# Performance work log

Measured on AMD Instinct MI355X. Metric: run time of the kernel, lower is better.

## Reference

```python
import jax, jax.numpy as jnp
import numpy as np


def setup_inputs() -> dict:
    key = jax.random.key(0)
    k1, k2 = jax.random.split(key)
    B, H, W, C = 16, 1024, 1024, 3
    image = jax.random.normal(k1, (B, H, W, C), dtype=jnp.float32)
    flow = jax.random.normal(k2, (B, H, W, 2), dtype=jnp.float32)
    return {"image": image, "flow": flow}


def reference(image, flow):
    # Backward warp: out(p) = bilinear_sample(image, p + flow(p)).
    # NOTE: the original build() swaps width/height (width=shape[1], height=shape[2]);
    # this is only consistent for square images (H == W), which we assume here.
    B, H, W, C = image.shape
    grid_x = jnp.arange(W, dtype=jnp.float32)[None, None, :]  # [1,1,W]
    grid_y = jnp.arange(H, dtype=jnp.float32)[None, :, None]  # [1,H,1]
    x = grid_x + flow[..., 0]  # [B,H,W]
    y = grid_y + flow[..., 1]
    # normalize to [-1,1] then back (faithful to original round-trip)
    x = 0.5 * (2.0 * (x / W - 0.5) + 1.0) * W
    y = 0.5 * (2.0 * (y / H - 0.5) + 1.0) * H
    # corner indices (tf.cast truncates toward zero, as does astype(int32))
    x0 = x.astype(jnp.int32)
    x1 = x0 + 1
    y0 = y.astype(jnp.int32)
    y1 = y0 + 1
    x0 = jnp.clip(x0, 0, W - 1)
    x1 = jnp.clip(x1, 0, W - 1)
    y0 = jnp.clip(y0, 0, H - 1)
    y1 = jnp.clip(y1, 0, H - 1)
    # flat gather indices into [B*H*W, C] image, matching the 4 tf.gather calls
    base = (jnp.arange(B, dtype=jnp.int32) * (H * W))[:, None, None]  # [B,1,1]
    flat_img = image.reshape(B * H * W, C)
    ia = (base + y0 * W + x0).reshape(-1)
    ib = (base + y1 * W + x0).reshape(-1)
    ic = (base + y0 * W + x1).reshape(-1)
    idd = (base + y1 * W + x1).reshape(-1)
    pa = flat_img[ia]  # [B*H*W, C]
    pb = flat_img[ib]
    pc = flat_img[ic]
    pd = flat_img[idd]
    # bilinear blend weights from clipped corner coords (as in original)
    x0f = x0.astype(jnp.float32).reshape(-1)
    x1f = x1.astype(jnp.float32).reshape(-1)
    y0f = y0.astype(jnp.float32).reshape(-1)
    y1f = y1.astype(jnp.float32).reshape(-1)
    xf = x.reshape(-1)
    yf = y.reshape(-1)
    wa = ((x1f - xf) * (y1f - yf))[:, None]
    wb = ((x1f - xf) * (yf - y0f))[:, None]
    wc = ((xf - x0f) * (y1f - yf))[:, None]
    wd = ((xf - x0f) * (yf - y0f))[:, None]
    out = wa * pa + wb * pb + wc * pc + wd * pd
    return out.reshape(B, H, W, C)
```

## Files before the change

### kernel.cpp

```cpp
#include <hip/hip_runtime.h>


struct __attribute__((packed, aligned(4))) R6 { float v[6]; };
typedef float f4 __attribute__((ext_vector_type(4), aligned(8)));
typedef float f2 __attribute__((ext_vector_type(2), aligned(8)));

__global__ __launch_bounds__(256) void backwarp_kernel(
    const float* __restrict__ image,
    const float* __restrict__ flow,
    float* __restrict__ out) {
  constexpr int H = 1024, W = 1024;
  constexpr int NB = 16384;
  constexpr int CHUNK = NB / 8;

  int bid = blockIdx.x;
  int sb = (bid & 7) * CHUNK + (bid >> 3);

  int b      = sb >> 10;
  int r      = sb & 1023;
  int tile_x = r >> 6;
  int tile_y = r & 63;

  int qx = threadIdx.x & 31;
  int qy = threadIdx.x >> 5;
  int w0 = (tile_x << 6) + (qx << 1);
  int h0 = (tile_y << 4) + (qy << 1);
  int plane = b << 20;

#pragma unroll
  for (int dy = 0; dy < 2; ++dy) {
    int h = h0 + dy;
    int idx0 = plane + (h << 10) + w0;
    f4 fl = __builtin_nontemporal_load(
        reinterpret_cast<const f4*>(flow + (size_t)idx0 * 2));
    float res[6];
#pragma unroll
    for (int dx = 0; dx < 2; ++dx) {
      float x = (float)(w0 + dx) + (dx ? fl.z : fl.x);
      float y = (float)h + (dx ? fl.w : fl.y);
      x = 0.5f * (2.0f * (x * (1.0f / W) - 0.5f) + 1.0f) * W;
      y = 0.5f * (2.0f * (y * (1.0f / H) - 0.5f) + 1.0f) * H;

      int x0 = (int)x;
      int y0 = (int)y;
      int x1 = x0 + 1;
      int y1 = y0 + 1;
      x0 = min(max(x0, 0), W - 1);
      x1 = min(max(x1, 0), W - 1);
      y0 = min(max(y0, 0), H - 1);
      y1 = min(max(y1, 0), H - 1);

      float wa = ((float)x1 - x) * ((float)y1 - y);
      float wb = ((float)x1 - x) * (y - (float)y0);
      float wc = (x - (float)x0) * ((float)y1 - y);
      float wd = (x - (float)x0) * (y - (float)y0);

      int bx = min(x0, W - 2);
      bool hiA = (x0 != bx);
      bool hiC = (x1 != bx);

      const R6 r0 = *reinterpret_cast<const R6*>(image + (size_t)(plane + (y0 << 10) + bx) * 3);
      const R6 r1 = *reinterpret_cast<const R6*>(image + (size_t)(plane + (y1 << 10) + bx) * 3);

#pragma unroll
      for (int c = 0; c < 3; ++c) {
        float pa  = hiA ? r0.v[3 + c] : r0.v[c];
        float pc_ = hiC ? r0.v[3 + c] : r0.v[c];
        float pb  = hiA ? r1.v[3 + c] : r1.v[c];
        float pd  = hiC ? r1.v[3 + c] : r1.v[c];
        res[dx * 3 + c] = wa * pa + wb * pb + wc * pc_ + wd * pd;
      }
    }
    float* o = out + (size_t)idx0 * 3;
    f4 s0 = {res[0], res[1], res[2], res[3]};
    f2 s1 = {res[4], res[5]};
    __builtin_nontemporal_store(s0, reinterpret_cast<f4*>(o));
    __builtin_nontemporal_store(s1, reinterpret_cast<f2*>(o + 4));
  }
}

extern "C" void kernel_launch(void* const* d_in, const int* in_sizes, int n_in,
                              void* d_out, int out_size, void* d_ws, size_t ws_size,
                              hipStream_t stream) {
  const float* image = (const float*)d_in[0];
  const float* flow  = (const float*)d_in[1];
  float* out = (float*)d_out;

  backwarp_kernel<<<16384, 256, 0, stream>>>(image, flow, out);
}
```

Baseline: 144.7 us.

## Stage image halo tile in LDS for bilinear gathers with global fallback

Each block first cooperatively loads a 32-row by 80-pixel halo region of the image around its 16x64 output tile into shared memory, then serves corner gathers from LDS when they fall inside it, falling back to global loads otherwise. This aims to replace scattered, uncoalesced global gathers with coalesced bulk loads, given that flow values are standard-normal so most samples stay near the pixel. It adds a prologue load of about 2.5x the tile's image footprint per block, a __syncthreads, 32KB of LDS per block that may reduce occupancy, and a divergent fallback path. Output stores also switch from nontemporal to regular stores.

```diff
diff --git a/kernel.cpp b/kernel.cpp
--- a/kernel.cpp
+++ b/kernel.cpp
@@ -4,6 +4,7 @@
 struct __attribute__((packed, aligned(4))) R6 { float v[6]; };
 typedef float f4 __attribute__((ext_vector_type(4), aligned(8)));
 typedef float f2 __attribute__((ext_vector_type(2), aligned(8)));
+typedef float f4u __attribute__((ext_vector_type(4), aligned(4)));
 
 __global__ __launch_bounds__(256) void backwarp_kernel(
     const float* __restrict__ image,
@@ -13,19 +14,40 @@
   constexpr int NB = 16384;
   constexpr int CHUNK = NB / 8;
 
+  __shared__ float lds[32 * 256];
+
   int bid = blockIdx.x;
   int sb = (bid & 7) * CHUNK + (bid >> 3);
-
   int b      = sb >> 10;
   int r      = sb & 1023;
   int tile_x = r >> 6;
   int tile_y = r & 63;
+  int w0t = tile_x << 6;
+  int h0t = tile_y << 4;
+  int plane = b << 20;
+  int r_lo = h0t - 8;
+
+  int kmin = (tile_x == 0) ? 6 : 0;
+  int khi  = (tile_x == 15) ? 54 : 60;
+#pragma unroll
+  for (int j = 0; j < 8; ++j) {
+    int lin = threadIdx.x + (j << 8);
+    int i = lin >> 6;
+    int k = lin & 63;
+    int gr = r_lo + i;
+    if (k >= kmin && k < khi && gr >= 0 && gr < H) {
+      const char* src = (const char*)image +
+          ((long long)(plane + (gr << 10) + w0t - 8) * 12) + (k << 4);
+      f4u val = *reinterpret_cast<const f4u*>(src);
+      *reinterpret_cast<f4*>((char*)lds + i * 1024 + (k << 4)) = val;
+    }
+  }
+  __syncthreads();
 
   int qx = threadIdx.x & 31;
   int qy = threadIdx.x >> 5;
-  int w0 = (tile_x << 6) + (qx << 1);
-  int h0 = (tile_y << 4) + (qy << 1);
-  int plane = b << 20;
+  int w0 = w0t + (qx << 1);
+  int h0 = h0t + (qy << 1);
 
 #pragma unroll
   for (int dy = 0; dy < 2; ++dy) {
@@ -59,23 +81,46 @@
       bool hiA = (x0 != bx);
       bool hiC = (x1 != bx);
 
-      const R6 r0 = *reinterpret_cast<const R6*>(image + (size_t)(plane + (y0 << 10) + bx) * 3);
-      const R6 r1 = *reinterpret_cast<const R6*>(image + (size_t)(plane + (y1 << 10) + bx) * 3);
+      int ly0 = y0 - r_lo;
+      int ly1 = y1 - r_lo;
+      int lx  = bx - (w0t - 8);
+      bool oob = ((unsigned)ly0 > 31u) | ((unsigned)ly1 > 31u) |
+                 ((unsigned)lx > 78u);
 
-#pragma unroll
-      for (int c = 0; c < 3; ++c) {
-        float pa  = hiA ? r0.v[3 + c] : r0.v[c];
-        float pc_ = hiC ? r0.v[3 + c] : r0.v[c];
-        float pb  = hiA ? r1.v[3 + c] : r1.v[c];
-        float pd  = hiC ? r1.v[3 + c] : r1.v[c];
-        res[dx * 3 + c] = wa * pa + wb * pb + wc * pc_ + wd * pd;
+      float a0, a1, a2, a3, a4, a5;
+      float c0, c1, c2, c3, c4, c5;
+      if (!oob) {
+        int d0 = (ly0 << 8) + lx * 3;
+        int d1 = (ly1 << 8) + lx * 3;
+        a0 = lds[d0];     a1 = lds[d0 + 1]; a2 = lds[d0 + 2];
+        a3 = lds[d0 + 3]; a4 = lds[d0 + 4]; a5 = lds[d0 + 5];
+        c0 = lds[d1];     c1 = lds[d1 + 1]; c2 = lds[d1 + 2];
+        c3 = lds[d1 + 3]; c4 = lds[d1 + 4]; c5 = lds[d1 + 5];
+      } else {
+        const R6 g0 = *reinterpret_cast<const R6*>(
+            image + (size_t)(plane + (y0 << 10) + bx) * 3);
+        const R6 g1 = *reinterpret_cast<const R6*>(
+            image + (size_t)(plane + (y1 << 10) + bx) * 3);
+        a0 = g0.v[0]; a1 = g0.v[1]; a2 = g0.v[2];
+        a3 = g0.v[3]; a4 = g0.v[4]; a5 = g0.v[5];
+        c0 = g1.v[0]; c1 = g1.v[1]; c2 = g1.v[2];
+        c3 = g1.v[3]; c4 = g1.v[4]; c5 = g1.v[5];
       }
+
+      float pa0 = hiA ? a3 : a0, pa1 = hiA ? a4 : a1, pa2 = hiA ? a5 : a2;
+      float pc0 = hiC ? a3 : a0, pc1 = hiC ? a4 : a1, pc2 = hiC ? a5 : a2;
+      float pb0 = hiA ? c3 : c0, pb1 = hiA ? c4 : c1, pb2 = hiA ? c5 : c2;
+      float pd0 = hiC ? c3 : c0, pd1 = hiC ? c4 : c1, pd2 = hiC ? c5 : c2;
+
+      res[dx * 3 + 0] = wa * pa0 + wb * pb0 + wc * pc0 + wd * pd0;
+      res[dx * 3 + 1] = wa * pa1 + wb * pb1 + wc * pc1 + wd * pd1;
+      res[dx * 3 + 2] = wa * pa2 + wb * pb2 + wc * pc2 + wd * pd2;
     }
     float* o = out + (size_t)idx0 * 3;
     f4 s0 = {res[0], res[1], res[2], res[3]};
     f2 s1 = {res[4], res[5]};
-    __builtin_nontemporal_store(s0, reinterpret_cast<f4*>(o));
-    __builtin_nontemporal_store(s1, reinterpret_cast<f2*>(o + 4));
+    *reinterpret_cast<f4*>(o) = s0;
+    *reinterpret_cast<f2*>(o + 4) = s1;
   }
 }
 
```

Measured after the change: 198.1 us. 1.37x slower.
